# Kernel optimization log

Measured on AMD Instinct MI355X. Metric: run time of the kernel, lower is better.

Reference implementation:

```python
import jax, jax.numpy as jnp
import numpy as np

B, H, W, C = 16, 56, 56, 512
HEADS, WS, SHIFT = 16, 7, 3
N = WS * WS            # tokens per window = 49
NW = (H // WS) * (W // WS)  # 64 windows per image
HID = 4 * C
EPS = 1e-5


def _rel_pos_index():
    coords = np.stack(np.meshgrid(np.arange(WS), np.arange(WS), indexing='ij'))  # (2,WS,WS)
    coords = coords.reshape(2, -1)                       # (2,N)
    rel = coords[:, :, None] - coords[:, None, :]        # (2,N,N)
    rel = rel.transpose(1, 2, 0).astype(np.int64)        # (N,N,2)
    rel[:, :, 0] += WS - 1
    rel[:, :, 1] += WS - 1
    rel[:, :, 0] *= 2 * WS - 1
    return rel.sum(-1)                                   # (N,N) in [0, (2WS-1)^2)


def _attn_mask():
    # standard Swin shifted-window mask
    img = np.zeros((H, W), dtype=np.int64)
    cnt = 0
    for hs in (slice(0, -WS), slice(-WS, -SHIFT), slice(-SHIFT, None)):
        for ws in (slice(0, -WS), slice(-WS, -SHIFT), slice(-SHIFT, None)):
            img[hs, ws] = cnt
            cnt += 1
    win = img.reshape(H // WS, WS, W // WS, WS).transpose(0, 2, 1, 3).reshape(NW, N)
    diff = win[:, None, :] - win[:, :, None]             # (NW,N,N)
    return np.where(diff != 0, -100.0, 0.0).astype(np.float32)


REL_IDX = _rel_pos_index()
MASK = _attn_mask()


def _ln(x, g, b):
    m = x.mean(-1, keepdims=True)
    v = ((x - m) ** 2).mean(-1, keepdims=True)
    return (x - m) * jax.lax.rsqrt(v + EPS) * g + b


def setup_inputs() -> dict:
    key = jax.random.key(0)
    ks = jax.random.split(key, 16)
    s = 0.02
    return {
        'x': jax.random.normal(ks[0], (B, H * W, C), jnp.float32),
        'norm1_g': jnp.ones((C,), jnp.float32),
        'norm1_b': jnp.zeros((C,), jnp.float32),
        'qkv_w': jax.random.normal(ks[1], (3 * C, C), jnp.float32) * s,
        'qkv_b': jnp.zeros((3 * C,), jnp.float32),
        'proj_w': jax.random.normal(ks[2], (C, C), jnp.float32) * s,
        'proj_b': jnp.zeros((C,), jnp.float32),
        'rpb': jax.random.normal(ks[3], ((2 * WS - 1) ** 2, HEADS), jnp.float32) * s,
        'norm2_g': jnp.ones((C,), jnp.float32),
        'norm2_b': jnp.zeros((C,), jnp.float32),
        'fc1_w': jax.random.normal(ks[4], (HID, C), jnp.float32) * s,
        'fc1_b': jnp.zeros((HID,), jnp.float32),
        'fc2_w': jax.random.normal(ks[5], (C, HID), jnp.float32) * s,
        'fc2_b': jnp.zeros((C,), jnp.float32),
    }


def reference(x, norm1_g, norm1_b, qkv_w, qkv_b, proj_w, proj_b, rpb,
              norm2_g, norm2_b, fc1_w, fc1_b, fc2_w, fc2_b):
    hd = C // HEADS
    scale = hd ** -0.5

    shortcut = x
    h = _ln(x, norm1_g, norm1_b).reshape(B, H, W, C)
    # cyclic shift
    h = jnp.roll(h, (-SHIFT, -SHIFT), axis=(1, 2))
    # window partition -> (B*NW, N, C)
    h = h.reshape(B, H // WS, WS, W // WS, WS, C).transpose(0, 1, 3, 2, 4, 5)
    h = h.reshape(B * NW, N, C)

    qkv = h @ qkv_w.T + qkv_b                            # (B*NW, N, 3C)
    qkv = qkv.reshape(B * NW, N, 3, HEADS, hd).transpose(2, 0, 3, 1, 4)
    q, k, v = qkv[0], qkv[1], qkv[2]                     # (B*NW, HEADS, N, hd)

    attn = jnp.einsum('whnd,whmd->whnm', q * scale, k)   # (B*NW, HEADS, N, N)
    bias = rpb[REL_IDX].transpose(2, 0, 1)               # (HEADS, N, N)
    attn = attn + bias[None]
    attn = attn.reshape(B, NW, HEADS, N, N) + jnp.asarray(MASK)[None, :, None]
    attn = jax.nn.softmax(attn.reshape(B * NW, HEADS, N, N), axis=-1)

    out = jnp.einsum('whnm,whmd->whnd', attn, v)         # (B*NW, HEADS, N, hd)
    out = out.transpose(0, 2, 1, 3).reshape(B * NW, N, C)
    out = out @ proj_w.T + proj_b

    # window reverse + reverse shift
    out = out.reshape(B, H // WS, W // WS, WS, WS, C).transpose(0, 1, 3, 2, 4, 5)
    out = out.reshape(B, H, W, C)
    out = jnp.roll(out, (SHIFT, SHIFT), axis=(1, 2)).reshape(B, H * W, C)

    x = shortcut + out
    m = _ln(x, norm2_g, norm2_b)
    m = jax.nn.gelu(m @ fc1_w.T + fc1_b, approximate=False) @ fc2_w.T + fc2_b
    return x + m
```

## Files before the change

### kernel.cpp

```cpp
#include <hip/hip_runtime.h>
#include <hip/hip_bf16.h>

typedef __bf16 bf16;
typedef __bf16 bf16x8 __attribute__((ext_vector_type(8)));
typedef __bf16 bf16x4 __attribute__((ext_vector_type(4)));
typedef __bf16 bf16x2 __attribute__((ext_vector_type(2)));
typedef float f32x4 __attribute__((ext_vector_type(4)));

#define M_TOK 50176

#define GLD16(dst, src) __builtin_amdgcn_global_load_lds( \
    (const __attribute__((address_space(1))) void*)(src), \
    (__attribute__((address_space(3))) void*)(dst), 16, 0, 0)

__global__ __launch_bounds__(256) void convert_w_kernel(
    const float* __restrict__ w0, const float* __restrict__ w1,
    const float* __restrict__ w2, const float* __restrict__ w3,
    bf16* __restrict__ dst)
{
    int blk = blockIdx.x;
    const float* src; size_t srel, drel;
    if (blk < 768)       { src = w0; srel = (size_t)blk * 1024;          drel = srel; }
    else if (blk < 1024) { src = w1; srel = (size_t)(blk - 768) * 1024;  drel = 786432 + srel; }
    else if (blk < 2048) { src = w2; srel = (size_t)(blk - 1024) * 1024; drel = 1048576 + srel; }
    else                 { src = w3; srel = (size_t)(blk - 2048) * 1024; drel = 2097152 + srel; }
    int i = threadIdx.x * 4;
    float4 v = *(const float4*)(src + srel + i);
    bf16* d = dst + drel + i;
    d[0] = (bf16)v.x; d[1] = (bf16)v.y; d[2] = (bf16)v.z; d[3] = (bf16)v.w;
}

__global__ __launch_bounds__(64) void bias_table_kernel(
    const float* __restrict__ rpb, float* __restrict__ bt)
{
    int tq = blockIdx.x;
    int type = tq / 784, r = tq - type * 784;
    int head = r / 49, q = r - head * 49;
    int k = threadIdx.x;
    float v;
    if (k < 49) {
        int yq = q / 7, xq = q - yq * 7;
        int yk = k / 7, xk = k - yk * 7;
        int ridx = (yq - yk + 6) * 13 + (xq - xk + 6);
        v = rpb[ridx * 16 + head];
        int th = type >> 1, tw = type & 1;
        int qid = 3 * (th ? (yq < 4 ? 1 : 2) : 0) + (tw ? (xq < 4 ? 1 : 2) : 0);
        int kid = 3 * (th ? (yk < 4 ? 1 : 2) : 0) + (tw ? (xk < 4 ? 1 : 2) : 0);
        if (qid != kid) v -= 100.f;
    } else {
        v = -1e9f;
    }
    bt[(size_t)tq * 64 + k] = v;
}

__global__ __launch_bounds__(256) void ln1_window_kernel(
    const float* __restrict__ x, const float* __restrict__ g, const float* __restrict__ bta,
    bf16* __restrict__ h)
{
    int t = blockIdx.x;
    int win = t / 49, n = t - win * 49;
    int bi = win >> 6, nw = win & 63;
    int wh = nw >> 3, ww = nw & 7;
    int ny = n / 7, nx = n - ny * 7;
    int r = wh * 7 + ny + 3; if (r >= 56) r -= 56;
    int c = ww * 7 + nx + 3; if (c >= 56) c -= 56;
    const float* xr = x + ((size_t)bi * 3136 + r * 56 + c) * 512;
    int tid = threadIdx.x;
    float v0 = xr[tid];
    float v1 = xr[tid + 256];
    float s = v0 + v1, ss = v0 * v0 + v1 * v1;
#pragma unroll
    for (int o = 32; o; o >>= 1) { s += __shfl_down(s, o, 64); ss += __shfl_down(ss, o, 64); }
    __shared__ float red[8];
    int wave = tid >> 6, lane = tid & 63;
    if (lane == 0) { red[wave] = s; red[4 + wave] = ss; }
    __syncthreads();
    float S = red[0] + red[1] + red[2] + red[3];
    float SS = red[4] + red[5] + red[6] + red[7];
    float mean = S * (1.f / 512.f);
    float var = SS * (1.f / 512.f) - mean * mean;
    float rstd = rsqrtf(var + 1e-5f);
    bf16* hr = h + (size_t)t * 512;
    hr[tid] = (bf16)((v0 - mean) * rstd * g[tid] + bta[tid]);
    hr[tid + 256] = (bf16)((v1 - mean) * rstd * g[tid + 256] + bta[tid + 256]);
}

template <int X1BF>
__global__ __launch_bounds__(256) void ln2_kernel(
    const void* __restrict__ x1, const float* __restrict__ g,
    const float* __restrict__ bta, bf16* __restrict__ outp)
{
    int t = blockIdx.x;
    int tid = threadIdx.x;
    float v0, v1;
    if constexpr (X1BF) {
        const bf16* xr = (const bf16*)x1 + (size_t)t * 512;
        v0 = (float)xr[tid]; v1 = (float)xr[tid + 256];
    } else {
        const float* xr = (const float*)x1 + (size_t)t * 512;
        v0 = xr[tid]; v1 = xr[tid + 256];
    }
    float s = v0 + v1, ss = v0 * v0 + v1 * v1;
#pragma unroll
    for (int o = 32; o; o >>= 1) { s += __shfl_down(s, o, 64); ss += __shfl_down(ss, o, 64); }
    __shared__ float red[8];
    int wave = tid >> 6, lane = tid & 63;
    if (lane == 0) { red[wave] = s; red[4 + wave] = ss; }
    __syncthreads();
    float S = red[0] + red[1] + red[2] + red[3];
    float SS = red[4] + red[5] + red[6] + red[7];
    float mean = S * (1.f / 512.f);
    float var = SS * (1.f / 512.f) - mean * mean;
    float rstd = rsqrtf(var + 1e-5f);
    bf16* hr = outp + (size_t)t * 512;
    hr[tid] = (bf16)((v0 - mean) * rstd * g[tid] + bta[tid]);
    hr[tid + 256] = (bf16)((v1 - mean) * rstd * g[tid + 256] + bta[tid + 256]);
}

template <int MODE, int K, int X1BF>
__global__ __launch_bounds__(256, 4) void gemm128b_kernel(
    const bf16* __restrict__ A, const bf16* __restrict__ Wt, const float* __restrict__ bias,
    void* __restrict__ outp, const void* __restrict__ extra, int N)
{
    __shared__ bf16 As[128][64];
    __shared__ bf16 Ws[128][64];
    constexpr int NT = K / 64;
    int gx = gridDim.x;
    int lin = blockIdx.y * gx + blockIdx.x;
    int q8 = (gx * gridDim.y) >> 3;
    int lin2 = (lin & 7) * q8 + (lin >> 3);
    int bn = lin2 % gx, bm = lin2 / gx;
    int tid = threadIdx.x;
    int w = tid >> 6, lane = tid & 63;
    int wm = w >> 1, wn = w & 1;
    int fr = lane & 15, fq = lane >> 4;
    int srow = lane >> 3;
    int scol = ((lane & 7) ^ srow) * 8;
    const bf16* gA = A + (size_t)(bm * 128 + w * 32 + srow) * K + scol;
    const bf16* gB = Wt + (size_t)(bn * 128 + w * 32 + srow) * K + scol;

    f32x4 acc[4][4];
    f32x4 z = {0.f, 0.f, 0.f, 0.f};
#pragma unroll
    for (int mf = 0; mf < 4; mf++)
#pragma unroll
        for (int nf = 0; nf < 4; nf++) acc[mf][nf] = z;

    for (int kt = 0; kt < NT; ++kt) {
        if (kt) {
            asm volatile("s_waitcnt lgkmcnt(0)" ::: "memory");
            asm volatile("s_barrier" ::: "memory");
        }
#pragma unroll
        for (int i = 0; i < 4; i++)
            GLD16(&As[w * 32 + i * 8][0], gA + (size_t)(i * 8) * K + kt * 64);
#pragma unroll
        for (int i = 0; i < 4; i++)
            GLD16(&Ws[w * 32 + i * 8][0], gB + (size_t)(i * 8) * K + kt * 64);
        asm volatile("s_waitcnt vmcnt(0)" ::: "memory");
        asm volatile("s_barrier" ::: "memory");
#pragma unroll
        for (int kh = 0; kh < 2; kh++) {
            bf16x8 aF[4], bF[4];
            int c = kh * 4 + fq;
#pragma unroll
            for (int f = 0; f < 4; f++) {
                aF[f] = *(const bf16x8*)&As[wm * 64 + f * 16 + fr][(c ^ (fr & 7)) * 8];
                bF[f] = *(const bf16x8*)&Ws[wn * 64 + f * 16 + fr][(c ^ (fr & 7)) * 8];
            }
#pragma unroll
            for (int mf = 0; mf < 4; mf++)
#pragma unroll
                for (int nf = 0; nf < 4; nf++)
                    acc[mf][nf] = __builtin_amdgcn_mfma_f32_16x16x32_bf16(bF[nf], aF[mf], acc[mf][nf], 0, 0, 0);
        }
    }

#pragma unroll
    for (int mf = 0; mf < 4; mf++) {
        int row = bm * 128 + wm * 64 + mf * 16 + fr;
        size_t rowbase;
        if constexpr (MODE == 2) {
            int win = row / 49, n = row - win * 49;
            int bi = win >> 6, nw = win & 63;
            int wh = nw >> 3, wwi = nw & 7;
            int ny = n / 7, nx = n - ny * 7;
            int rr = wh * 7 + ny + 3; if (rr >= 56) rr -= 56;
            int cc = wwi * 7 + nx + 3; if (cc >= 56) cc -= 56;
            rowbase = ((size_t)bi * 3136 + rr * 56 + cc) * 512;
        } else {
            rowbase = (size_t)row * (MODE == 3 ? 512 : N);
        }
#pragma unroll
        for (int nf = 0; nf < 4; nf++) {
            int colb = bn * 128 + wn * 64 + nf * 16 + fq * 4;
            float4 b4 = *(const float4*)(bias + colb);
            float v0 = acc[mf][nf][0] + b4.x;
            float v1 = acc[mf][nf][1] + b4.y;
            float v2 = acc[mf][nf][2] + b4.z;
            float v3 = acc[mf][nf][3] + b4.w;
            size_t dst = rowbase + colb;
            if constexpr (MODE == 0) {
                bf16x4 t = {(bf16)v0, (bf16)v1, (bf16)v2, (bf16)v3};
                *(bf16x4*)((bf16*)outp + dst) = t;
            } else if constexpr (MODE == 1) {
                v0 = 0.5f * v0 * (1.f + erff(v0 * 0.70710678118654752f));
                v1 = 0.5f * v1 * (1.f + erff(v1 * 0.70710678118654752f));
                v2 = 0.5f * v2 * (1.f + erff(v2 * 0.70710678118654752f));
                v3 = 0.5f * v3 * (1.f + erff(v3 * 0.70710678118654752f));
                bf16x4 t = {(bf16)v0, (bf16)v1, (bf16)v2, (bf16)v3};
                *(bf16x4*)((bf16*)outp + dst) = t;
            } else if constexpr (MODE == 2) {
                float4 e = *(const float4*)((const float*)extra + dst);
                v0 += e.x; v1 += e.y; v2 += e.z; v3 += e.w;
                if constexpr (X1BF) {
                    bf16x4 t = {(bf16)v0, (bf16)v1, (bf16)v2, (bf16)v3};
                    *(bf16x4*)((bf16*)outp + dst) = t;
                } else {
                    float4 t = {v0, v1, v2, v3};
                    *(float4*)((float*)outp + dst) = t;
                }
            } else {
                if constexpr (X1BF) {
                    bf16x4 e = *(const bf16x4*)((const bf16*)extra + dst);
                    v0 += (float)e[0]; v1 += (float)e[1]; v2 += (float)e[2]; v3 += (float)e[3];
                } else {
                    float4 e = *(const float4*)((const float*)extra + dst);
                    v0 += e.x; v1 += e.y; v2 += e.z; v3 += e.w;
                }
                float4 t = {v0, v1, v2, v3};
                *(float4*)((float*)outp + dst) = t;
            }
        }
    }
}

__global__ __launch_bounds__(64) void attn_mfma_kernel(
    const bf16* __restrict__ qkv, const float* __restrict__ bt, bf16* __restrict__ outp)
{
    int wid0 = blockIdx.x;
    int wid = (wid0 & 7) * 2048 + (wid0 >> 3);
    int win = wid >> 4, head = wid & 15;
    int nw = win & 63;
    int type = ((nw >> 3) == 7 ? 2 : 0) + ((nw & 7) == 7 ? 1 : 0);
    int lane = threadIdx.x;
    int fr = lane & 15, fq = lane >> 4;
    __shared__ bf16 Vt[32][72];
    __shared__ bf16 Ps[64][72];
    const bf16* base = qkv + (size_t)win * 49 * 1536;

    uint4 z4 = {0, 0, 0, 0};
#pragma unroll
    for (int c = lane; c < 288; c += 64) ((uint4*)Vt)[c] = z4;
    __syncthreads();
    for (int c = lane; c < 1568; c += 64) {
        int tok = c >> 5, d = c & 31;
        Vt[d][tok] = base[(size_t)tok * 1536 + 1024 + head * 32 + d];
    }
    bf16x8 qf[4], kf[4];
#pragma unroll
    for (int i = 0; i < 4; i++) {
        int tq = i * 16 + fr; if (tq > 48) tq = 48;
        qf[i] = *(const bf16x8*)(base + (size_t)tq * 1536 + head * 32 + fq * 8);
        kf[i] = *(const bf16x8*)(base + (size_t)tq * 1536 + 512 + head * 32 + fq * 8);
    }
    f32x4 z = {0.f, 0.f, 0.f, 0.f};
    f32x4 st[4][4];
#pragma unroll
    for (int mi = 0; mi < 4; mi++)
#pragma unroll
        for (int ni = 0; ni < 4; ni++)
            st[mi][ni] = __builtin_amdgcn_mfma_f32_16x16x32_bf16(kf[mi], qf[ni], z, 0, 0, 0);
    __syncthreads();

    const float* btb = bt + (size_t)(type * 16 + head) * 49 * 64;
    float p[4][4][4];
    float inv[4];
#pragma unroll
    for (int ni = 0; ni < 4; ni++) {
        int q = ni * 16 + fr; if (q > 48) q = 48;
        const float* btr = btb + q * 64;
        float m = -1e30f;
#pragma unroll
        for (int mi = 0; mi < 4; mi++) {
            float4 bv = *(const float4*)(btr + mi * 16 + fq * 4);
#pragma unroll
            for (int r = 0; r < 4; r++) {
                float s = st[mi][ni][r] * 0.17677669529663689f + (&bv.x)[r];
                p[mi][ni][r] = s;
                m = fmaxf(m, s);
            }
        }
        m = fmaxf(m, __shfl_xor(m, 16));
        m = fmaxf(m, __shfl_xor(m, 32));
        float sum = 0.f;
#pragma unroll
        for (int mi = 0; mi < 4; mi++)
#pragma unroll
            for (int r = 0; r < 4; r++) {
                float e = __expf(p[mi][ni][r] - m);
                p[mi][ni][r] = e;
                sum += e;
            }
        sum += __shfl_xor(sum, 16);
        sum += __shfl_xor(sum, 32);
        inv[ni] = 1.f / sum;
    }
#pragma unroll
    for (int mi = 0; mi < 4; mi++)
#pragma unroll
        for (int ni = 0; ni < 4; ni++) {
            bf16x4 t;
            t[0] = (bf16)p[mi][ni][0]; t[1] = (bf16)p[mi][ni][1];
            t[2] = (bf16)p[mi][ni][2]; t[3] = (bf16)p[mi][ni][3];
            *(bf16x4*)&Ps[ni * 16 + fr][mi * 16 + fq * 4] = t;
        }
    __syncthreads();
    f32x4 o[2][4];
#pragma unroll
    for (int mi = 0; mi < 2; mi++)
#pragma unroll
        for (int ni = 0; ni < 4; ni++) o[mi][ni] = z;
#pragma unroll
    for (int kt = 0; kt < 2; kt++) {
        bf16x8 a0 = *(const bf16x8*)&Vt[fr][kt * 32 + fq * 8];
        bf16x8 a1 = *(const bf16x8*)&Vt[16 + fr][kt * 32 + fq * 8];
#pragma unroll
        for (int ni = 0; ni < 4; ni++) {
            bf16x8 b = *(const bf16x8*)&Ps[ni * 16 + fr][kt * 32 + fq * 8];
            o[0][ni] = __builtin_amdgcn_mfma_f32_16x16x32_bf16(a0, b, o[0][ni], 0, 0, 0);
            o[1][ni] = __builtin_amdgcn_mfma_f32_16x16x32_bf16(a1, b, o[1][ni], 0, 0, 0);
        }
    }
#pragma unroll
    for (int ni = 0; ni < 4; ni++) {
        int q = ni * 16 + fr;
        if (q < 49) {
            bf16* orow = outp + (size_t)(win * 49 + q) * 512 + head * 32;
#pragma unroll
            for (int mi = 0; mi < 2; mi++)
#pragma unroll
                for (int r2 = 0; r2 < 2; r2++) {
                    bf16x2 t;
                    t[0] = (bf16)(o[mi][ni][2 * r2] * inv[ni]);
                    t[1] = (bf16)(o[mi][ni][2 * r2 + 1] * inv[ni]);
                    *(bf16x2*)(orow + mi * 16 + fq * 4 + 2 * r2) = t;
                }
        }
    }
}

extern "C" void kernel_launch(void* const* d_in, const int* in_sizes, int n_in,
                              void* d_out, int out_size, void* d_ws, size_t ws_size,
                              hipStream_t stream)
{
    const float* x      = (const float*)d_in[0];
    const float* n1g    = (const float*)d_in[1];
    const float* n1b    = (const float*)d_in[2];
    const float* qkv_w  = (const float*)d_in[3];
    const float* qkv_b  = (const float*)d_in[4];
    const float* proj_w = (const float*)d_in[5];
    const float* proj_b = (const float*)d_in[6];
    const float* rpb    = (const float*)d_in[7];
    const float* n2g    = (const float*)d_in[8];
    const float* n2b    = (const float*)d_in[9];
    const float* fc1_w  = (const float*)d_in[10];
    const float* fc1_b  = (const float*)d_in[11];
    const float* fc2_w  = (const float*)d_in[12];
    const float* fc2_b  = (const float*)d_in[13];

    char* ws = (char*)d_ws;
    bf16* qkv  = (bf16*)ws;
    bf16* h    = (bf16*)(ws + 154140672ull);
    float* bt  = (float*)(ws + 154140672ull);
    bf16* ao   = (bf16*)(ws + 205520896ull);
    bf16* wbuf = (bf16*)(ws + 256901120ull);
    bf16* hid  = (bf16*)ws;
    bf16* ln2h = ao;
    bf16* wq  = wbuf;
    bf16* wp  = wbuf + 786432;
    bf16* wf1 = wbuf + 1048576;
    bf16* wf2 = wbuf + 2097152;

    bool xb = (ws_size >= 314572800ull);
    void* x1 = xb ? (void*)(ws + 263192576ull) : (void*)d_out;

    convert_w_kernel<<<3072, 256, 0, stream>>>(qkv_w, proj_w, fc1_w, fc2_w, wbuf);
    ln1_window_kernel<<<M_TOK, 256, 0, stream>>>(x, n1g, n1b, h);
    gemm128b_kernel<0, 512, 0><<<dim3(12, 392), 256, 0, stream>>>(h, wq, qkv_b, qkv, nullptr, 1536);
    bias_table_kernel<<<3136, 64, 0, stream>>>(rpb, bt);
    attn_mfma_kernel<<<16384, 64, 0, stream>>>(qkv, bt, ao);
    if (xb) {
        gemm128b_kernel<2, 512, 1><<<dim3(4, 392), 256, 0, stream>>>(ao, wp, proj_b, x1, x, 512);
        ln2_kernel<1><<<M_TOK, 256, 0, stream>>>(x1, n2g, n2b, ln2h);
        gemm128b_kernel<1, 512, 1><<<dim3(16, 392), 256, 0, stream>>>(ln2h, wf1, fc1_b, hid, nullptr, 2048);
        gemm128b_kernel<3, 2048, 1><<<dim3(4, 392), 256, 0, stream>>>(hid, wf2, fc2_b, d_out, x1, 512);
    } else {
        gemm128b_kernel<2, 512, 0><<<dim3(4, 392), 256, 0, stream>>>(ao, wp, proj_b, x1, x, 512);
        ln2_kernel<0><<<M_TOK, 256, 0, stream>>>(x1, n2g, n2b, ln2h);
        gemm128b_kernel<1, 512, 0><<<dim3(16, 392), 256, 0, stream>>>(ln2h, wf1, fc1_b, hid, nullptr, 2048);
        gemm128b_kernel<3, 2048, 0><<<dim3(4, 392), 256, 0, stream>>>(hid, wf2, fc2_b, d_out, x1, 512);
    }
}
```

Measured before the change: 583.6 us.

## Double-buffer GEMM LDS tiles with register prefetch and use tanh GELU

The GEMM kernel now uses two LDS buffers for the A and W tiles. The global-to-LDS load for tile kt+2 is issued while MFMAs run on the current tile, and the fragment reads for the next k-half are prefetched into a second register set. This is meant to hide global-load latency and cut the per-tile barrier stalls, at the cost of twice the LDS per block and a lower occupancy hint (2 blocks instead of 4). The fc1 epilogue also swaps the exact erf GELU for a tanh approximation built on __expf, which is cheaper but slightly changes the numerics.

```diff
diff --git a/kernel.cpp b/kernel.cpp
--- a/kernel.cpp
+++ b/kernel.cpp
@@ -117,13 +117,30 @@
     hr[tid + 256] = (bf16)((v1 - mean) * rstd * g[tid + 256] + bta[tid + 256]);
 }
 
+#define LDSREAD(set, buf, kh) do { \
+    int c_ = (kh) * 4 + fq; \
+    _Pragma("unroll") \
+    for (int f = 0; f < 4; f++) { \
+        aF[set][f] = *(const bf16x8*)&As[buf][wm * 64 + f * 16 + fr][((c_) ^ (fr & 7)) * 8]; \
+        bF[set][f] = *(const bf16x8*)&Ws[buf][wn * 64 + f * 16 + fr][((c_) ^ (fr & 7)) * 8]; \
+    } \
+} while (0)
+
+#define MFMASET(set) do { \
+    _Pragma("unroll") \
+    for (int mf = 0; mf < 4; mf++) \
+        _Pragma("unroll") \
+        for (int nf = 0; nf < 4; nf++) \
+            acc[mf][nf] = __builtin_amdgcn_mfma_f32_16x16x32_bf16(bF[set][nf], aF[set][mf], acc[mf][nf], 0, 0, 0); \
+} while (0)
+
 template <int MODE, int K, int X1BF>
-__global__ __launch_bounds__(256, 4) void gemm128b_kernel(
+__global__ __launch_bounds__(256, 2) void gemm128p_kernel(
     const bf16* __restrict__ A, const bf16* __restrict__ Wt, const float* __restrict__ bias,
     void* __restrict__ outp, const void* __restrict__ extra, int N)
 {
-    __shared__ bf16 As[128][64];
-    __shared__ bf16 Ws[128][64];
+    __shared__ bf16 As[2][128][64];
+    __shared__ bf16 Ws[2][128][64];
     constexpr int NT = K / 64;
     int gx = gridDim.x;
     int lin = blockIdx.y * gx + blockIdx.x;
@@ -146,34 +163,33 @@
 #pragma unroll
         for (int nf = 0; nf < 4; nf++) acc[mf][nf] = z;
 
+    auto STAGE_ = [&](int b, int kt) {
+#pragma unroll
+        for (int i = 0; i < 4; i++)
+            GLD16(&As[b][w * 32 + i * 8][0], gA + (size_t)(i * 8) * K + kt * 64);
+#pragma unroll
+        for (int i = 0; i < 4; i++)
+            GLD16(&Ws[b][w * 32 + i * 8][0], gB + (size_t)(i * 8) * K + kt * 64);
+    };
+
+    bf16x8 aF[2][4], bF[2][4];
+
+    STAGE_(0, 0);
+    STAGE_(1, 1);
+    asm volatile("s_waitcnt vmcnt(8)" ::: "memory");
+    __builtin_amdgcn_s_barrier();
+    LDSREAD(0, 0, 0);
+
     for (int kt = 0; kt < NT; ++kt) {
-        if (kt) {
-            asm volatile("s_waitcnt lgkmcnt(0)" ::: "memory");
-            asm volatile("s_barrier" ::: "memory");
-        }
-#pragma unroll
-        for (int i = 0; i < 4; i++)
-            GLD16(&As[w * 32 + i * 8][0], gA + (size_t)(i * 8) * K + kt * 64);
-#pragma unroll
-        for (int i = 0; i < 4; i++)
-            GLD16(&Ws[w * 32 + i * 8][0], gB + (size_t)(i * 8) * K + kt * 64);
+        int cur = kt & 1;
+        LDSREAD(1, cur, 1);
+        MFMASET(0);
+        asm volatile("s_waitcnt lgkmcnt(0)" ::: "memory");
         asm volatile("s_waitcnt vmcnt(0)" ::: "memory");
-        asm volatile("s_barrier" ::: "memory");
-#pragma unroll
-        for (int kh = 0; kh < 2; kh++) {
-            bf16x8 aF[4], bF[4];
-            int c = kh * 4 + fq;
-#pragma unroll
-            for (int f = 0; f < 4; f++) {
-                aF[f] = *(const bf16x8*)&As[wm * 64 + f * 16 + fr][(c ^ (fr & 7)) * 8];
-                bF[f] = *(const bf16x8*)&Ws[wn * 64 + f * 16 + fr][(c ^ (fr & 7)) * 8];
-            }
-#pragma unroll
-            for (int mf = 0; mf < 4; mf++)
-#pragma unroll
-                for (int nf = 0; nf < 4; nf++)
-                    acc[mf][nf] = __builtin_amdgcn_mfma_f32_16x16x32_bf16(bF[nf], aF[mf], acc[mf][nf], 0, 0, 0);
-        }
+        __builtin_amdgcn_s_barrier();
+        if (kt + 2 < NT) STAGE_(cur, kt + 2);
+        MFMASET(1);
+        if (kt + 1 < NT) LDSREAD(0, cur ^ 1, 0);
     }
 
 #pragma unroll
@@ -204,10 +220,16 @@
                 bf16x4 t = {(bf16)v0, (bf16)v1, (bf16)v2, (bf16)v3};
                 *(bf16x4*)((bf16*)outp + dst) = t;
             } else if constexpr (MODE == 1) {
-                v0 = 0.5f * v0 * (1.f + erff(v0 * 0.70710678118654752f));
-                v1 = 0.5f * v1 * (1.f + erff(v1 * 0.70710678118654752f));
-                v2 = 0.5f * v2 * (1.f + erff(v2 * 0.70710678118654752f));
-                v3 = 0.5f * v3 * (1.f + erff(v3 * 0.70710678118654752f));
+#pragma unroll
+                for (int j = 0; j < 4; j++) {
+                    float* vp = (j == 0) ? &v0 : (j == 1) ? &v1 : (j == 2) ? &v2 : &v3;
+                    float xv = *vp;
+                    float y = 0.7978845608028654f * (xv + 0.044715f * xv * xv * xv);
+                    float u = __expf(-2.f * fabsf(y));
+                    float th = (1.f - u) / (1.f + u);
+                    th = (y < 0.f) ? -th : th;
+                    *vp = 0.5f * xv * (1.f + th);
+                }
                 bf16x4 t = {(bf16)v0, (bf16)v1, (bf16)v2, (bf16)v3};
                 *(bf16x4*)((bf16*)outp + dst) = t;
             } else if constexpr (MODE == 2) {
@@ -387,18 +409,18 @@
 
     convert_w_kernel<<<3072, 256, 0, stream>>>(qkv_w, proj_w, fc1_w, fc2_w, wbuf);
     ln1_window_kernel<<<M_TOK, 256, 0, stream>>>(x, n1g, n1b, h);
-    gemm128b_kernel<0, 512, 0><<<dim3(12, 392), 256, 0, stream>>>(h, wq, qkv_b, qkv, nullptr, 1536);
+    gemm128p_kernel<0, 512, 0><<<dim3(12, 392), 256, 0, stream>>>(h, wq, qkv_b, qkv, nullptr, 1536);
     bias_table_kernel<<<3136, 64, 0, stream>>>(rpb, bt);
     attn_mfma_kernel<<<16384, 64, 0, stream>>>(qkv, bt, ao);
     if (xb) {
-        gemm128b_kernel<2, 512, 1><<<dim3(4, 392), 256, 0, stream>>>(ao, wp, proj_b, x1, x, 512);
+        gemm128p_kernel<2, 512, 1><<<dim3(4, 392), 256, 0, stream>>>(ao, wp, proj_b, x1, x, 512);
         ln2_kernel<1><<<M_TOK, 256, 0, stream>>>(x1, n2g, n2b, ln2h);
-        gemm128b_kernel<1, 512, 1><<<dim3(16, 392), 256, 0, stream>>>(ln2h, wf1, fc1_b, hid, nullptr, 2048);
-        gemm128b_kernel<3, 2048, 1><<<dim3(4, 392), 256, 0, stream>>>(hid, wf2, fc2_b, d_out, x1, 512);
+        gemm128p_kernel<1, 512, 1><<<dim3(16, 392), 256, 0, stream>>>(ln2h, wf1, fc1_b, hid, nullptr, 2048);
+        gemm128p_kernel<3, 2048, 1><<<dim3(4, 392), 256, 0, stream>>>(hid, wf2, fc2_b, d_out, x1, 512);
     } else {
-        gemm128b_kernel<2, 512, 0><<<dim3(4, 392), 256, 0, stream>>>(ao, wp, proj_b, x1, x, 512);
+        gemm128p_kernel<2, 512, 0><<<dim3(4, 392), 256, 0, stream>>>(ao, wp, proj_b, x1, x, 512);
         ln2_kernel<0><<<M_TOK, 256, 0, stream>>>(x1, n2g, n2b, ln2h);
-        gemm128b_kernel<1, 512, 0><<<dim3(16, 392), 256, 0, stream>>>(ln2h, wf1, fc1_b, hid, nullptr, 2048);
-        gemm128b_kernel<3, 2048, 0><<<dim3(4, 392), 256, 0, stream>>>(hid, wf2, fc2_b, d_out, x1, 512);
-    }
-}
+        gemm128p_kernel<1, 512, 0><<<dim3(16, 392), 256, 0, stream>>>(ln2h, wf1, fc1_b, hid, nullptr, 2048);
+        gemm128p_kernel<3, 2048, 0><<<dim3(4, 392), 256, 0, stream>>>(hid, wf2, fc2_b, d_out, x1, 512);
+    }
+}
```

Result: slower. 704.5 us (+20.7%).

## Replace 128x128 GEMM with double-buffered 256x256 tile, 8-wave pipelined schedule

Applied to the files above, without the earlier changes.

Every linear layer now uses a new GEMM kernel with 256x256 output tiles, 512 threads (8 waves) and double-buffered LDS. Global-to-LDS loads for later k-steps are interleaved with four quadrant MFMA phases, and MFMA sections get raised priority. The aim is more data reuse per loaded byte and overlap of memory traffic with matrix math, in place of the old load-wait-compute loop. In exchange, occupancy drops to one block per CU with 128KB of LDS, and the barrier and vmcnt bookkeeping is fragile.

```diff
diff --git a/kernel.cpp b/kernel.cpp
--- a/kernel.cpp
+++ b/kernel.cpp
@@ -117,14 +117,39 @@
     hr[tid + 256] = (bf16)((v1 - mean) * rstd * g[tid + 256] + bta[tid + 256]);
 }
 
+#define BAR() asm volatile("s_barrier" ::: "memory")
+#define LGKM0() asm volatile("s_waitcnt lgkmcnt(0)" ::: "memory")
+
+#define RDA(bb_, mh_) do { \
+  _Pragma("unroll") for (int i_ = 0; i_ < 4; i_++) \
+    _Pragma("unroll") for (int kh_ = 0; kh_ < 2; kh_++) \
+      aF[i_][kh_] = *(const bf16x8*)&LA[bb_][wm][(mh_) * 64 + i_ * 16 + fr][((kh_ * 4 + fq) ^ (fr & 7)) * 8]; \
+} while (0)
+
+#define RDB(dst_, bb_, nh_) do { \
+  _Pragma("unroll") for (int i_ = 0; i_ < 2; i_++) \
+    _Pragma("unroll") for (int kh_ = 0; kh_ < 2; kh_++) \
+      dst_[i_][kh_] = *(const bf16x8*)&LB[bb_][wn >> 1][(wn & 1) * 64 + (nh_) * 32 + i_ * 16 + fr][((kh_ * 4 + fq) ^ (fr & 7)) * 8]; \
+} while (0)
+
+#define MM(mh_, nh_, B_) do { \
+  __builtin_amdgcn_s_setprio(1); \
+  _Pragma("unroll") for (int i_ = 0; i_ < 4; i_++) \
+    _Pragma("unroll") for (int j_ = 0; j_ < 2; j_++) \
+      _Pragma("unroll") for (int kh_ = 0; kh_ < 2; kh_++) \
+        acc[(mh_) * 4 + i_][(nh_) * 2 + j_] = __builtin_amdgcn_mfma_f32_16x16x32_bf16( \
+            B_[j_][kh_], aF[i_][kh_], acc[(mh_) * 4 + i_][(nh_) * 2 + j_], 0, 0, 0); \
+  __builtin_amdgcn_s_setprio(0); \
+} while (0)
+
 template <int MODE, int K, int X1BF>
-__global__ __launch_bounds__(256, 4) void gemm128b_kernel(
+__global__ __launch_bounds__(512, 1) void gemm256_kernel(
     const bf16* __restrict__ A, const bf16* __restrict__ Wt, const float* __restrict__ bias,
     void* __restrict__ outp, const void* __restrict__ extra, int N)
 {
-    __shared__ bf16 As[128][64];
-    __shared__ bf16 Ws[128][64];
     constexpr int NT = K / 64;
+    __shared__ bf16 LA[2][2][128][64];
+    __shared__ bf16 LB[2][2][128][64];
     int gx = gridDim.x;
     int lin = blockIdx.y * gx + blockIdx.x;
     int q8 = (gx * gridDim.y) >> 3;
@@ -132,53 +157,67 @@
     int bn = lin2 % gx, bm = lin2 / gx;
     int tid = threadIdx.x;
     int w = tid >> 6, lane = tid & 63;
-    int wm = w >> 1, wn = w & 1;
+    int wm = w >> 2, wn = w & 3;
     int fr = lane & 15, fq = lane >> 4;
     int srow = lane >> 3;
-    int scol = ((lane & 7) ^ srow) * 8;
-    const bf16* gA = A + (size_t)(bm * 128 + w * 32 + srow) * K + scol;
-    const bf16* gB = Wt + (size_t)(bn * 128 + w * 32 + srow) * K + scol;
-
-    f32x4 acc[4][4];
+    int schunk = ((lane & 7) ^ srow) * 8;
+    const bf16* gA = A + (size_t)(bm * 256 + w * 8 + srow) * K + schunk;
+    const bf16* gB = Wt + (size_t)(bn * 256 + w * 8 + srow) * K + schunk;
+
+    f32x4 acc[8][4];
     f32x4 z = {0.f, 0.f, 0.f, 0.f};
 #pragma unroll
-    for (int mf = 0; mf < 4; mf++)
-#pragma unroll
-        for (int nf = 0; nf < 4; nf++) acc[mf][nf] = z;
-
+    for (int i = 0; i < 8; i++)
+#pragma unroll
+        for (int j = 0; j < 4; j++) acc[i][j] = z;
+
+    auto stA = [&](int bb, int hf, int kt) {
+        const bf16* s = gA + (size_t)(hf * 128) * K + kt * 64;
+        GLD16(&LA[bb][hf][w * 8][0], s);
+        GLD16(&LA[bb][hf][w * 8 + 64][0], s + (size_t)64 * K);
+    };
+    auto stB = [&](int bb, int hf, int kt) {
+        const bf16* s = gB + (size_t)(hf * 128) * K + kt * 64;
+        GLD16(&LB[bb][hf][w * 8][0], s);
+        GLD16(&LB[bb][hf][w * 8 + 64][0], s + (size_t)64 * K);
+    };
+
+    stA(0, 0, 0); stB(0, 0, 0); stA(0, 1, 0); stB(0, 1, 0);
+    stA(1, 0, 1); stB(1, 0, 1); stA(1, 1, 1);
+    asm volatile("s_waitcnt vmcnt(6)" ::: "memory");
+    BAR();
+
+    bf16x8 aF[4][2], bB0[2][2], bB1[2][2];
     for (int kt = 0; kt < NT; ++kt) {
-        if (kt) {
-            asm volatile("s_waitcnt lgkmcnt(0)" ::: "memory");
-            asm volatile("s_barrier" ::: "memory");
-        }
-#pragma unroll
-        for (int i = 0; i < 4; i++)
-            GLD16(&As[w * 32 + i * 8][0], gA + (size_t)(i * 8) * K + kt * 64);
-#pragma unroll
-        for (int i = 0; i < 4; i++)
-            GLD16(&Ws[w * 32 + i * 8][0], gB + (size_t)(i * 8) * K + kt * 64);
-        asm volatile("s_waitcnt vmcnt(0)" ::: "memory");
-        asm volatile("s_barrier" ::: "memory");
-#pragma unroll
-        for (int kh = 0; kh < 2; kh++) {
-            bf16x8 aF[4], bF[4];
-            int c = kh * 4 + fq;
-#pragma unroll
-            for (int f = 0; f < 4; f++) {
-                aF[f] = *(const bf16x8*)&As[wm * 64 + f * 16 + fr][(c ^ (fr & 7)) * 8];
-                bF[f] = *(const bf16x8*)&Ws[wn * 64 + f * 16 + fr][(c ^ (fr & 7)) * 8];
-            }
-#pragma unroll
-            for (int mf = 0; mf < 4; mf++)
-#pragma unroll
-                for (int nf = 0; nf < 4; nf++)
-                    acc[mf][nf] = __builtin_amdgcn_mfma_f32_16x16x32_bf16(bF[nf], aF[mf], acc[mf][nf], 0, 0, 0);
-        }
-    }
-
-#pragma unroll
-    for (int mf = 0; mf < 4; mf++) {
-        int row = bm * 128 + wm * 64 + mf * 16 + fr;
+        int bb = kt & 1;
+        RDA(bb, 0); RDB(bB0, bb, 0);
+        if (kt + 1 < NT) stB(bb ^ 1, 1, kt + 1);
+        BAR(); LGKM0();
+        MM(0, 0, bB0);
+        BAR();
+        RDB(bB1, bb, 1);
+        BAR(); LGKM0();
+        MM(0, 1, bB1);
+        BAR();
+        RDA(bb, 1);
+        if (kt + 2 < NT) stB(bb, 0, kt + 2);
+        BAR(); LGKM0();
+        MM(1, 1, bB1);
+        BAR();
+        if (kt + 2 < NT) {
+            stA(bb, 0, kt + 2); stA(bb, 1, kt + 2);
+            asm volatile("s_waitcnt vmcnt(6)" ::: "memory");
+        } else {
+            asm volatile("s_waitcnt vmcnt(0)" ::: "memory");
+        }
+        BAR();
+        MM(1, 0, bB0);
+        BAR();
+    }
+
+#pragma unroll
+    for (int mf = 0; mf < 8; mf++) {
+        int row = bm * 256 + wm * 128 + mf * 16 + fr;
         size_t rowbase;
         if constexpr (MODE == 2) {
             int win = row / 49, n = row - win * 49;
@@ -193,7 +232,7 @@
         }
 #pragma unroll
         for (int nf = 0; nf < 4; nf++) {
-            int colb = bn * 128 + wn * 64 + nf * 16 + fq * 4;
+            int colb = bn * 256 + wn * 64 + nf * 16 + fq * 4;
             float4 b4 = *(const float4*)(bias + colb);
             float v0 = acc[mf][nf][0] + b4.x;
             float v1 = acc[mf][nf][1] + b4.y;
@@ -387,18 +426,18 @@
 
     convert_w_kernel<<<3072, 256, 0, stream>>>(qkv_w, proj_w, fc1_w, fc2_w, wbuf);
     ln1_window_kernel<<<M_TOK, 256, 0, stream>>>(x, n1g, n1b, h);
-    gemm128b_kernel<0, 512, 0><<<dim3(12, 392), 256, 0, stream>>>(h, wq, qkv_b, qkv, nullptr, 1536);
+    gemm256_kernel<0, 512, 0><<<dim3(6, 196), 512, 0, stream>>>(h, wq, qkv_b, qkv, nullptr, 1536);
     bias_table_kernel<<<3136, 64, 0, stream>>>(rpb, bt);
     attn_mfma_kernel<<<16384, 64, 0, stream>>>(qkv, bt, ao);
     if (xb) {
-        gemm128b_kernel<2, 512, 1><<<dim3(4, 392), 256, 0, stream>>>(ao, wp, proj_b, x1, x, 512);
+        gemm256_kernel<2, 512, 1><<<dim3(2, 196), 512, 0, stream>>>(ao, wp, proj_b, x1, x, 512);
         ln2_kernel<1><<<M_TOK, 256, 0, stream>>>(x1, n2g, n2b, ln2h);
-        gemm128b_kernel<1, 512, 1><<<dim3(16, 392), 256, 0, stream>>>(ln2h, wf1, fc1_b, hid, nullptr, 2048);
-        gemm128b_kernel<3, 2048, 1><<<dim3(4, 392), 256, 0, stream>>>(hid, wf2, fc2_b, d_out, x1, 512);
+        gemm256_kernel<1, 512, 1><<<dim3(8, 196), 512, 0, stream>>>(ln2h, wf1, fc1_b, hid, nullptr, 2048);
+        gemm256_kernel<3, 2048, 1><<<dim3(2, 196), 512, 0, stream>>>(hid, wf2, fc2_b, d_out, x1, 512);
     } else {
-        gemm128b_kernel<2, 512, 0><<<dim3(4, 392), 256, 0, stream>>>(ao, wp, proj_b, x1, x, 512);
+        gemm256_kernel<2, 512, 0><<<dim3(2, 196), 512, 0, stream>>>(ao, wp, proj_b, x1, x, 512);
         ln2_kernel<0><<<M_TOK, 256, 0, stream>>>(x1, n2g, n2b, ln2h);
-        gemm128b_kernel<1, 512, 0><<<dim3(16, 392), 256, 0, stream>>>(ln2h, wf1, fc1_b, hid, nullptr, 2048);
-        gemm128b_kernel<3, 2048, 0><<<dim3(4, 392), 256, 0, stream>>>(hid, wf2, fc2_b, d_out, x1, 512);
-    }
-}
+        gemm256_kernel<1, 512, 0><<<dim3(8, 196), 512, 0, stream>>>(ln2h, wf1, fc1_b, hid, nullptr, 2048);
+        gemm256_kernel<3, 2048, 0><<<dim3(2, 196), 512, 0, stream>>>(hid, wf2, fc2_b, d_out, x1, 512);
+    }
+}
```

After: 805.5 us. 1.38x slower.
